# Performance work log

Measured on AMD Instinct MI355X. Metric: run time of the kernel, lower is better.

Reference implementation:

```python
import jax, jax.numpy as jnp
import numpy as np

IMG = 8       # image_size
LH = 150      # l_h
LQ = 10       # l_q
K = 10        # value-iteration steps
B = 16384     # batch
N_STATES = 2 + IMG * IMG


def _conv(x, w, pad):
    # NCHW conv, stride 1
    return jax.lax.conv_general_dilated(
        x, w, window_strides=(1, 1), padding=[(pad, pad), (pad, pad)],
        dimension_numbers=('NCHW', 'OIHW', 'NCHW'))


def setup_inputs() -> dict:
    key = jax.random.key(0)
    ks = jax.random.split(key, 8)
    grid = jax.random.normal(ks[0], (B, IMG * IMG), dtype=jnp.float32)
    pos = jax.random.randint(ks[1], (B, 2), 0, IMG).astype(jnp.float32)
    S = jnp.concatenate([grid, pos], axis=1)                      # [B, 66]
    Wh = jax.random.normal(ks[2], (LH, 1, 3, 3), jnp.float32) * 0.1
    bh = jnp.zeros((LH,), jnp.float32)
    Wr = jax.random.normal(ks[3], (1, LH, 1, 1), jnp.float32) * 0.1
    Wq = jax.random.normal(ks[4], (LQ, 1, 3, 3), jnp.float32) * 0.1
    w = jax.random.normal(ks[5], (LQ, 1, 3, 3), jnp.float32) * 0.1
    Wfc = jax.random.normal(ks[6], (8, LQ), jnp.float32) * 0.1
    return {'S': S, 'Wh': Wh, 'bh': bh, 'Wr': Wr, 'Wq': Wq, 'w': w, 'Wfc': Wfc}


def reference(S, Wh, bh, Wr, Wq, w, Wfc):
    X = S[:, :IMG * IMG].reshape(-1, 1, IMG, IMG)                 # [B,1,8,8]
    s1 = S[:, IMG * IMG].astype(jnp.int32)                        # row index
    s2 = S[:, IMG * IMG + 1].astype(jnp.int32)                    # col index

    h = _conv(X, Wh, 1) + bh[None, :, None, None]                 # [B,150,8,8]
    r = _conv(h, Wr, 0)                                           # [B,1,8,8]
    q = _conv(r, Wq, 1)                                           # [B,10,8,8]
    v = jnp.max(q, axis=1, keepdims=True)                         # [B,1,8,8]

    Wcat = jnp.concatenate([Wq, w], axis=1)                       # [10,2,3,3]

    def step(v, _):
        qq = _conv(jnp.concatenate([r, v], axis=1), Wcat, 1)
        return jnp.max(qq, axis=1, keepdims=True), None

    v, _ = jax.lax.scan(step, v, None, length=K - 1)
    q = _conv(jnp.concatenate([r, v], axis=1), Wcat, 1)           # [B,10,8,8]

    bidx = jnp.arange(q.shape[0])
    q_sel = q[bidx, :, s1, s2]                                    # [B,10]
    logits = q_sel @ Wfc.T                                        # [B,8]
    return logits
```

## Files before the change

### kernel.cpp

```cpp
#include <hip/hip_runtime.h>

#define IMG 8
#define LH 150
#define LQ 10
#define KITER 10
#define ROW (IMG * IMG + 2)

__device__ __forceinline__ float bperm(int byte_addr, float v) {
    return __builtin_bit_cast(float,
        __builtin_amdgcn_ds_bpermute(byte_addr, __builtin_bit_cast(int, v)));
}

__device__ __forceinline__ float max10(const float q[LQ]) {
    const float g0 = fmaxf(fmaxf(q[0], q[1]), q[2]);
    const float g1 = fmaxf(fmaxf(q[3], q[4]), q[5]);
    const float g2 = fmaxf(fmaxf(q[6], q[7]), q[8]);
    return fmaxf(fmaxf(g0, g1), fmaxf(g2, q[9]));
}

__global__ void weff_kernel(const float* __restrict__ Wh,
                            const float* __restrict__ bh,
                            const float* __restrict__ Wr,
                            float* __restrict__ ws) {
    const int wv = threadIdx.x >> 6;
    const int lane = threadIdx.x & 63;
    float partial = 0.f;
    for (int c = lane; c < LH; c += 64) {
        const float wr = Wr[c];
        partial += wr * ((wv < 9) ? Wh[c * 9 + wv] : bh[c]);
    }
    #pragma unroll
    for (int off = 32; off > 0; off >>= 1)
        partial += __shfl_xor(partial, off);
    if (lane == 0) ws[wv] = partial;
}

__global__ __launch_bounds__(256, 2) void vin_kernel(
    const float* __restrict__ S,
    const float* __restrict__ Wq,
    const float* __restrict__ w,
    const float* __restrict__ Wfc,
    const float* __restrict__ ws,
    float* __restrict__ out,
    int B) {
    const int wave = threadIdx.x >> 6;
    const int lane = threadIdx.x & 63;
    const long b0 = (long)(blockIdx.x * 4 + wave) * 2;
    if (b0 >= B) return;

    const int y = lane >> 3, x = lane & 7;

    int   addr[9];
    float msk[9];
    #pragma unroll
    for (int t = 0; t < 9; ++t) {
        const int dy = t / 3 - 1, dx = t % 3 - 1;
        const int ny = y + dy, nx = x + dx;
        const bool v = ((unsigned)ny < 8u) && ((unsigned)nx < 8u);
        addr[t] = (v ? (ny * 8 + nx) : 0) << 2;
        msk[t]  = v ? 1.f : 0.f;
    }

    float wreg[LQ][9];
    #pragma unroll
    for (int o = 0; o < LQ; ++o)
        #pragma unroll
        for (int t = 0; t < 9; ++t)
            wreg[o][t] = w[o * 9 + t] * msk[t];

    const float* S0 = S + b0 * ROW;
    const float X0 = S0[lane];
    const float X1 = S0[ROW + lane];
    const int sel0 = ((int)S0[IMG * IMG] * 8 + (int)S0[IMG * IMG + 1]) << 2;
    const int sel1 = ((int)S0[ROW + IMG * IMG] * 8 + (int)S0[ROW + IMG * IMG + 1]) << 2;

    float r0 = ws[9], r1 = ws[9];
    #pragma unroll
    for (int t = 0; t < 9; ++t) {
        const float wm = ws[t] * msk[t];
        r0 = fmaf(wm, bperm(addr[t], X0), r0);
        r1 = fmaf(wm, bperm(addr[t], X1), r1);
    }

    float qr0[LQ], qr1[LQ];
    #pragma unroll
    for (int t = 0; t < 9; ++t) {
        const float a0 = bperm(addr[t], r0) * msk[t];
        const float a1 = bperm(addr[t], r1) * msk[t];
        #pragma unroll
        for (int o = 0; o < LQ; ++o) {
            const float wq = Wq[o * 9 + t];
            if (t == 0) { qr0[o] = a0 * wq; qr1[o] = a1 * wq; }
            else        { qr0[o] = fmaf(a0, wq, qr0[o]);
                          qr1[o] = fmaf(a1, wq, qr1[o]); }
        }
    }

    float v0 = max10(qr0), v1 = max10(qr1);

    #pragma unroll
    for (int k = 0; k < KITER - 1; ++k) {
        float vn0[9], vn1[9];
        #pragma unroll
        for (int t = 0; t < 9; ++t) {
            vn0[t] = bperm(addr[t], v0);
            vn1[t] = bperm(addr[t], v1);
        }
        float m0, m1;
        #pragma unroll
        for (int o = 0; o < LQ; ++o) {
            float acc0 = qr0[o], acc1 = qr1[o];
            #pragma unroll
            for (int t = 0; t < 9; ++t) {
                acc0 = fmaf(vn0[t], wreg[o][t], acc0);
                acc1 = fmaf(vn1[t], wreg[o][t], acc1);
            }
            if (o == 0) { m0 = acc0; m1 = acc1; }
            else        { m0 = fmaxf(m0, acc0); m1 = fmaxf(m1, acc1); }
        }
        v0 = m0; v1 = m1;
    }

    float qs0[LQ], qs1[LQ];
    {
        float vn0[9], vn1[9];
        #pragma unroll
        for (int t = 0; t < 9; ++t) {
            vn0[t] = bperm(addr[t], v0);
            vn1[t] = bperm(addr[t], v1);
        }
        #pragma unroll
        for (int o = 0; o < LQ; ++o) {
            float acc0 = qr0[o], acc1 = qr1[o];
            #pragma unroll
            for (int t = 0; t < 9; ++t) {
                acc0 = fmaf(vn0[t], wreg[o][t], acc0);
                acc1 = fmaf(vn1[t], wreg[o][t], acc1);
            }
            qs0[o] = bperm(sel0, acc0);
            qs1[o] = bperm(sel1, acc1);
        }
    }

    if (lane < 16) {
        const int row = lane & 7;
        float acc = 0.f;
        #pragma unroll
        for (int o = 0; o < LQ; ++o)
            acc = fmaf((lane < 8) ? qs0[o] : qs1[o], Wfc[row * LQ + o], acc);
        out[b0 * 8 + lane] = acc;
    }
}

extern "C" void kernel_launch(void* const* d_in, const int* in_sizes, int n_in,
                              void* d_out, int out_size, void* d_ws, size_t ws_size,
                              hipStream_t stream) {
    const float* S   = (const float*)d_in[0];
    const float* Wh  = (const float*)d_in[1];
    const float* bh  = (const float*)d_in[2];
    const float* Wr  = (const float*)d_in[3];
    const float* Wq  = (const float*)d_in[4];
    const float* w   = (const float*)d_in[5];
    const float* Wfc = (const float*)d_in[6];
    float* out = (float*)d_out;
    float* ws  = (float*)d_ws;

    const int B = in_sizes[0] / ROW;

    weff_kernel<<<1, 640, 0, stream>>>(Wh, bh, Wr, ws);

    const int grid = (B + 7) / 8;
    vin_kernel<<<grid, 256, 0, stream>>>(S, Wq, w, Wfc, ws, out, B);
}
```

Measured before the change: 94.99 us.

## Remap each image onto 32 lanes and use DPP/swizzle stencil instead of bpermute

Each image now occupies 32 lanes holding two rows each, and the 3x3 stencil neighbours come from DPP row shifts and ds_swizzle instead of nine ds_bpermute calls per value. The separate weff kernel is dropped: every wave recomputes the collapsed Wh·Wr weights with shuffle reductions, which removes one launch. Weights move to scalar registers through readfirstlane, the iteration loop is no longer unrolled, and launch bounds are raised to allow more waves per SIMD. The trade is redundant per-wave work on the 150-channel weight reduction, and the more complex lane mapping carries a correctness risk.

```diff
diff --git a/kernel.cpp b/kernel.cpp
--- a/kernel.cpp
+++ b/kernel.cpp
@@ -11,36 +11,35 @@
         __builtin_amdgcn_ds_bpermute(byte_addr, __builtin_bit_cast(int, v)));
 }
 
-__device__ __forceinline__ float max10(const float q[LQ]) {
-    const float g0 = fmaxf(fmaxf(q[0], q[1]), q[2]);
-    const float g1 = fmaxf(fmaxf(q[3], q[4]), q[5]);
-    const float g2 = fmaxf(fmaxf(q[6], q[7]), q[8]);
-    return fmaxf(fmaxf(g0, g1), fmaxf(g2, q[9]));
-}
-
-__global__ void weff_kernel(const float* __restrict__ Wh,
-                            const float* __restrict__ bh,
-                            const float* __restrict__ Wr,
-                            float* __restrict__ ws) {
-    const int wv = threadIdx.x >> 6;
-    const int lane = threadIdx.x & 63;
-    float partial = 0.f;
-    for (int c = lane; c < LH; c += 64) {
-        const float wr = Wr[c];
-        partial += wr * ((wv < 9) ? Wh[c * 9 + wv] : bh[c]);
-    }
-    #pragma unroll
-    for (int off = 32; off > 0; off >>= 1)
-        partial += __shfl_xor(partial, off);
-    if (lane == 0) ws[wv] = partial;
-}
-
-__global__ __launch_bounds__(256, 2) void vin_kernel(
+__device__ __forceinline__ float rfl(float v) {
+    return __builtin_bit_cast(float,
+        __builtin_amdgcn_readfirstlane(__builtin_bit_cast(int, v)));
+}
+
+__device__ __forceinline__ float swz24(float v) {
+    return __builtin_bit_cast(float,
+        __builtin_amdgcn_ds_swizzle(__builtin_bit_cast(int, v), 0x601F));
+}
+
+template <int CTRL>
+__device__ __forceinline__ float dppf(float v) {
+    return __builtin_bit_cast(float,
+        __builtin_amdgcn_update_dpp(0, __builtin_bit_cast(int, v),
+                                    CTRL, 0xF, 0xF, true));
+}
+#define DPP_SHR1 0x111
+#define DPP_SHL1 0x101
+#define DPP_SHR8 0x118
+#define DPP_SHL8 0x108
+
+__global__ __launch_bounds__(256, 8) void vin_kernel(
     const float* __restrict__ S,
+    const float* __restrict__ Wh,
+    const float* __restrict__ bh,
+    const float* __restrict__ Wr,
     const float* __restrict__ Wq,
     const float* __restrict__ w,
     const float* __restrict__ Wfc,
-    const float* __restrict__ ws,
     float* __restrict__ out,
     int B) {
     const int wave = threadIdx.x >> 6;
@@ -48,108 +47,167 @@
     const long b0 = (long)(blockIdx.x * 4 + wave) * 2;
     if (b0 >= B) return;
 
-    const int y = lane >> 3, x = lane & 7;
-
-    int   addr[9];
-    float msk[9];
-    #pragma unroll
-    for (int t = 0; t < 9; ++t) {
-        const int dy = t / 3 - 1, dx = t % 3 - 1;
-        const int ny = y + dy, nx = x + dx;
-        const bool v = ((unsigned)ny < 8u) && ((unsigned)nx < 8u);
-        addr[t] = (v ? (ny * 8 + nx) : 0) << 2;
-        msk[t]  = v ? 1.f : 0.f;
-    }
-
-    float wreg[LQ][9];
+    const int item = lane >> 5;
+    const int l32  = lane & 31;
+    const int h    = l32 >> 4;
+    const int q    = (l32 >> 3) & 1;
+    const int x    = l32 & 7;
+
+    const float mskL = (x > 0) ? 1.f : 0.f;
+    const float mskR = (x < 7) ? 1.f : 0.f;
+    const float m3   = (h == 1 && q == 0) ? 1.f : 0.f;
+    const float m4   = (h == 0 && q == 1) ? 1.f : 0.f;
+
+    float p[10];
+    #pragma unroll
+    for (int t = 0; t < 10; ++t) p[t] = 0.f;
+    for (int c = lane; c < LH; c += 64) {
+        const float wr = Wr[c];
+        #pragma unroll
+        for (int t = 0; t < 9; ++t) p[t] = fmaf(wr, Wh[c * 9 + t], p[t]);
+        p[9] = fmaf(wr, bh[c], p[9]);
+    }
+    #pragma unroll
+    for (int t = 0; t < 10; ++t)
+        #pragma unroll
+        for (int off = 32; off > 0; off >>= 1)
+            p[t] += __shfl_xor(p[t], off);
+
+    const long b = b0 + item;
+    const float* Sb = S + b * ROW;
+    float v[2];
+    v[0] = Sb[(h * 4 + q) * 8 + x];
+    v[1] = Sb[(h * 4 + 2 + q) * 8 + x];
+    const int s1i = (int)Sb[IMG * IMG];
+    const int s2i = (int)Sb[IMG * IMG + 1];
+    const int selAddr = ((item << 5) + ((s1i >> 2) << 4) + ((s1i & 1) << 3) + s2i) << 2;
+    const float e0 = (((s1i >> 1) & 1) == 0) ? 1.f : 0.f;
+    const float e1 = 1.f - e0;
+
+    auto rows5 = [&](const float vv[2], float d[5]) {
+        const float X3 = swz24(vv[1]);
+        const float X4 = swz24(vv[0]);
+        d[1] = vv[0];
+        d[3] = vv[1];
+        d[2] = dppf<DPP_SHL8>(vv[0]) + dppf<DPP_SHR8>(vv[1]);
+        d[0] = fmaf(X3, m3, dppf<DPP_SHR8>(vv[0]));
+        d[4] = fmaf(X4, m4, dppf<DPP_SHL8>(vv[1]));
+    };
+    auto lcr = [&](const float d[5], float L[5], float R[5]) {
+        #pragma unroll
+        for (int j = 0; j < 5; ++j) {
+            L[j] = mskL * dppf<DPP_SHR1>(d[j]);
+            R[j] = mskR * dppf<DPP_SHL1>(d[j]);
+        }
+    };
+
+    {
+        float d[5], L[5], R[5];
+        rows5(v, d); lcr(d, L, R);
+        const float bias = p[9];
+        #pragma unroll
+        for (int r = 0; r < 2; ++r) {
+            float a = bias;
+            #pragma unroll
+            for (int ky = 0; ky < 3; ++ky) {
+                const int j = 2 * r + ky;
+                a = fmaf(L[j], p[ky * 3 + 0], a);
+                a = fmaf(d[j], p[ky * 3 + 1], a);
+                a = fmaf(R[j], p[ky * 3 + 2], a);
+            }
+            v[r] = a;
+        }
+    }
+
+    float qr[LQ][2];
+    {
+        float d[5], L[5], R[5];
+        rows5(v, d); lcr(d, L, R);
+        #pragma unroll
+        for (int o = 0; o < LQ; ++o)
+            #pragma unroll
+            for (int r = 0; r < 2; ++r) {
+                float a = L[2 * r] * Wq[o * 9 + 0];
+                a = fmaf(d[2 * r],     Wq[o * 9 + 1], a);
+                a = fmaf(R[2 * r],     Wq[o * 9 + 2], a);
+                a = fmaf(L[2 * r + 1], Wq[o * 9 + 3], a);
+                a = fmaf(d[2 * r + 1], Wq[o * 9 + 4], a);
+                a = fmaf(R[2 * r + 1], Wq[o * 9 + 5], a);
+                a = fmaf(L[2 * r + 2], Wq[o * 9 + 6], a);
+                a = fmaf(d[2 * r + 2], Wq[o * 9 + 7], a);
+                a = fmaf(R[2 * r + 2], Wq[o * 9 + 8], a);
+                qr[o][r] = a;
+            }
+    }
+
+    float wu[LQ][9];
     #pragma unroll
     for (int o = 0; o < LQ; ++o)
         #pragma unroll
         for (int t = 0; t < 9; ++t)
-            wreg[o][t] = w[o * 9 + t] * msk[t];
-
-    const float* S0 = S + b0 * ROW;
-    const float X0 = S0[lane];
-    const float X1 = S0[ROW + lane];
-    const int sel0 = ((int)S0[IMG * IMG] * 8 + (int)S0[IMG * IMG + 1]) << 2;
-    const int sel1 = ((int)S0[ROW + IMG * IMG] * 8 + (int)S0[ROW + IMG * IMG + 1]) << 2;
-
-    float r0 = ws[9], r1 = ws[9];
-    #pragma unroll
-    for (int t = 0; t < 9; ++t) {
-        const float wm = ws[t] * msk[t];
-        r0 = fmaf(wm, bperm(addr[t], X0), r0);
-        r1 = fmaf(wm, bperm(addr[t], X1), r1);
-    }
-
-    float qr0[LQ], qr1[LQ];
-    #pragma unroll
-    for (int t = 0; t < 9; ++t) {
-        const float a0 = bperm(addr[t], r0) * msk[t];
-        const float a1 = bperm(addr[t], r1) * msk[t];
+            wu[o][t] = rfl(w[o * 9 + t]);
+
+    #pragma unroll
+    for (int r = 0; r < 2; ++r) {
+        const float g0 = fmaxf(fmaxf(qr[0][r], qr[1][r]), qr[2][r]);
+        const float g1 = fmaxf(fmaxf(qr[3][r], qr[4][r]), qr[5][r]);
+        const float g2 = fmaxf(fmaxf(qr[6][r], qr[7][r]), qr[8][r]);
+        v[r] = fmaxf(fmaxf(g0, g1), fmaxf(g2, qr[9][r]));
+    }
+
+    #pragma unroll 1
+    for (int k = 0; k < KITER - 1; ++k) {
+        float d[5], L[5], R[5];
+        rows5(v, d); lcr(d, L, R);
+        float m[2];
+        #pragma unroll
+        for (int o = 0; o < LQ; ++o)
+            #pragma unroll
+            for (int r = 0; r < 2; ++r) {
+                float a = qr[o][r];
+                a = fmaf(L[2 * r],     wu[o][0], a);
+                a = fmaf(d[2 * r],     wu[o][1], a);
+                a = fmaf(R[2 * r],     wu[o][2], a);
+                a = fmaf(L[2 * r + 1], wu[o][3], a);
+                a = fmaf(d[2 * r + 1], wu[o][4], a);
+                a = fmaf(R[2 * r + 1], wu[o][5], a);
+                a = fmaf(L[2 * r + 2], wu[o][6], a);
+                a = fmaf(d[2 * r + 2], wu[o][7], a);
+                a = fmaf(R[2 * r + 2], wu[o][8], a);
+                m[r] = (o == 0) ? a : fmaxf(m[r], a);
+            }
+        v[0] = m[0]; v[1] = m[1];
+    }
+
+    const int row = l32 & 7;
+    float osum = 0.f;
+    {
+        float d[5], L[5], R[5];
+        rows5(v, d); lcr(d, L, R);
         #pragma unroll
         for (int o = 0; o < LQ; ++o) {
-            const float wq = Wq[o * 9 + t];
-            if (t == 0) { qr0[o] = a0 * wq; qr1[o] = a1 * wq; }
-            else        { qr0[o] = fmaf(a0, wq, qr0[o]);
-                          qr1[o] = fmaf(a1, wq, qr1[o]); }
+            float a0, a1;
+            #pragma unroll
+            for (int r = 0; r < 2; ++r) {
+                float a = qr[o][r];
+                a = fmaf(L[2 * r],     wu[o][0], a);
+                a = fmaf(d[2 * r],     wu[o][1], a);
+                a = fmaf(R[2 * r],     wu[o][2], a);
+                a = fmaf(L[2 * r + 1], wu[o][3], a);
+                a = fmaf(d[2 * r + 1], wu[o][4], a);
+                a = fmaf(R[2 * r + 1], wu[o][5], a);
+                a = fmaf(L[2 * r + 2], wu[o][6], a);
+                a = fmaf(d[2 * r + 2], wu[o][7], a);
+                a = fmaf(R[2 * r + 2], wu[o][8], a);
+                if (r == 0) a0 = a; else a1 = a;
+            }
+            float t = a0 * e0;
+            t = fmaf(a1, e1, t);
+            const float qs = bperm(selAddr, t);
+            osum = fmaf(qs, Wfc[row * LQ + o], osum);
         }
     }
-
-    float v0 = max10(qr0), v1 = max10(qr1);
-
-    #pragma unroll
-    for (int k = 0; k < KITER - 1; ++k) {
-        float vn0[9], vn1[9];
-        #pragma unroll
-        for (int t = 0; t < 9; ++t) {
-            vn0[t] = bperm(addr[t], v0);
-            vn1[t] = bperm(addr[t], v1);
-        }
-        float m0, m1;
-        #pragma unroll
-        for (int o = 0; o < LQ; ++o) {
-            float acc0 = qr0[o], acc1 = qr1[o];
-            #pragma unroll
-            for (int t = 0; t < 9; ++t) {
-                acc0 = fmaf(vn0[t], wreg[o][t], acc0);
-                acc1 = fmaf(vn1[t], wreg[o][t], acc1);
-            }
-            if (o == 0) { m0 = acc0; m1 = acc1; }
-            else        { m0 = fmaxf(m0, acc0); m1 = fmaxf(m1, acc1); }
-        }
-        v0 = m0; v1 = m1;
-    }
-
-    float qs0[LQ], qs1[LQ];
-    {
-        float vn0[9], vn1[9];
-        #pragma unroll
-        for (int t = 0; t < 9; ++t) {
-            vn0[t] = bperm(addr[t], v0);
-            vn1[t] = bperm(addr[t], v1);
-        }
-        #pragma unroll
-        for (int o = 0; o < LQ; ++o) {
-            float acc0 = qr0[o], acc1 = qr1[o];
-            #pragma unroll
-            for (int t = 0; t < 9; ++t) {
-                acc0 = fmaf(vn0[t], wreg[o][t], acc0);
-                acc1 = fmaf(vn1[t], wreg[o][t], acc1);
-            }
-            qs0[o] = bperm(sel0, acc0);
-            qs1[o] = bperm(sel1, acc1);
-        }
-    }
-
-    if (lane < 16) {
-        const int row = lane & 7;
-        float acc = 0.f;
-        #pragma unroll
-        for (int o = 0; o < LQ; ++o)
-            acc = fmaf((lane < 8) ? qs0[o] : qs1[o], Wfc[row * LQ + o], acc);
-        out[b0 * 8 + lane] = acc;
-    }
+    if (l32 < 8) out[b * 8 + row] = osum;
 }
 
 extern "C" void kernel_launch(void* const* d_in, const int* in_sizes, int n_in,
@@ -163,12 +221,10 @@
     const float* w   = (const float*)d_in[5];
     const float* Wfc = (const float*)d_in[6];
     float* out = (float*)d_out;
-    float* ws  = (float*)d_ws;
+    (void)d_ws; (void)ws_size;
 
     const int B = in_sizes[0] / ROW;
 
-    weff_kernel<<<1, 640, 0, stream>>>(Wh, bh, Wr, ws);
-
     const int grid = (B + 7) / 8;
-    vin_kernel<<<grid, 256, 0, stream>>>(S, Wq, w, Wfc, ws, out, B);
-}
+    vin_kernel<<<grid, 256, 0, stream>>>(S, Wh, bh, Wr, Wq, w, Wfc, out, B);
+}
```

Measured after the change: 110.6 us. 1.16x slower.
